# Kernel optimization log

Hardware: AMD Instinct MI355X
Metric: run time of the kernel (lower is better)

Reference implementation:

```python
import jax, jax.numpy as jnp
import numpy as np

DIM = 1024
HEADS = 16

def setup_inputs() -> dict:
    key = jax.random.key(0)
    k1, k2 = jax.random.split(key)
    x = jax.random.normal(k1, (4, 2048, DIM), dtype=jnp.float32)
    # torch nn.Linear(dim, 3*dim, bias=False): weight shape [3*dim, dim], y = x @ W.T
    W_qkv = jax.random.normal(k2, (3 * DIM, DIM), dtype=jnp.float32) * (DIM ** -0.5)
    return {"x": x, "W_qkv": W_qkv}

def reference(x, W_qkv):
    B, N, D = x.shape
    H = HEADS
    hd = D // H
    scale = hd ** -0.5
    qkv = jnp.einsum('bnd,ed->bne', x, W_qkv)            # [B,N,3D]
    qkv = qkv.reshape(B, N, 3, H, hd).transpose(2, 0, 3, 1, 4)  # [3,B,H,N,hd]
    q, k, v = qkv[0], qkv[1], qkv[2]
    attn = jnp.einsum('bhnd,bhmd->bhnm', q, k) * scale   # [B,H,N,N]
    attn = jax.nn.softmax(attn, axis=-1)                 # dropout is identity at eval
    out = jnp.einsum('bhnm,bhmd->bhnd', attn, v)         # [B,H,N,hd]
    return out.transpose(0, 2, 1, 3).reshape(B, N, D)
```

## Files before the change

kernel.cpp:

```cpp
#include <hip/hip_runtime.h>

typedef unsigned short ushort_t;
typedef short bf16x8 __attribute__((ext_vector_type(8)));
typedef float f32x4 __attribute__((ext_vector_type(4)));
typedef float f32x16 __attribute__((ext_vector_type(16)));

__device__ __forceinline__ unsigned f2bf(float f) {
  union { float f; unsigned u; } v; v.f = f;
  return (v.u + 0x7FFFu + ((v.u >> 16) & 1u)) >> 16;
}

__device__ __forceinline__ void gll16(const void* g, const void* l) {
  __builtin_amdgcn_global_load_lds(
      (const __attribute__((address_space(1))) void*)g,
      (__attribute__((address_space(3))) void*)l, 16, 0, 0);
}

__global__ __launch_bounds__(256) void cvt_bf16(const float* __restrict__ src,
                                                ushort_t* __restrict__ dst, int n4) {
  int i = blockIdx.x * 256 + threadIdx.x;
  if (i >= n4) return;
  float4 v = ((const float4*)src)[i];
  uint2 o;
  o.x = f2bf(v.x) | (f2bf(v.y) << 16);
  o.y = f2bf(v.z) | (f2bf(v.w) << 16);
  ((uint2*)dst)[i] = o;
}

__global__ __launch_bounds__(256) void gemm_qkv(const ushort_t* __restrict__ A,
                                                const ushort_t* __restrict__ Bw,
                                                ushort_t* __restrict__ C) {
  __shared__ ushort_t As[128 * 64];
  __shared__ ushort_t Bs[128 * 64];
  const int tid = threadIdx.x;
  const int w = tid >> 6, ln = tid & 63;
  const int g = ln >> 4, lr = ln & 15;
  const int bx = blockIdx.x;
  const int nt = bx % 24, mt = bx / 24;
  const int m0 = mt * 128, n0 = nt * 128;
  const int wr = w >> 1, wc = w & 1;
  const float cscale = (nt < 8) ? 0.18033688f : 1.0f;

  f32x4 acc[4][4] = {};

  for (int kt = 0; kt < 16; ++kt) {
#pragma unroll
    for (int q = 0; q < 4; ++q) {
      int chunk = w * 256 + q * 64 + ln;
      int r = chunk >> 3, c = chunk & 7;
      int cs = c ^ (r & 7);
      gll16(A + (size_t)(m0 + r) * 1024 + kt * 64 + cs * 8, As + chunk * 8);
      gll16(Bw + (size_t)(n0 + r) * 1024 + kt * 64 + cs * 8, Bs + chunk * 8);
    }
    __syncthreads();
#pragma unroll
    for (int ks = 0; ks < 2; ++ks) {
      bf16x8 af[4], bfr[4];
#pragma unroll
      for (int mi = 0; mi < 4; ++mi) {
        int row = wr * 64 + mi * 16 + lr;
        af[mi] = *(const bf16x8*)((const char*)As + row * 128 +
                                  ((g * 16 + ks * 64) ^ ((row & 7) << 4)));
      }
#pragma unroll
      for (int ni = 0; ni < 4; ++ni) {
        int row = wc * 64 + ni * 16 + lr;
        bfr[ni] = *(const bf16x8*)((const char*)Bs + row * 128 +
                                   ((g * 16 + ks * 64) ^ ((row & 7) << 4)));
      }
#pragma unroll
      for (int mi = 0; mi < 4; ++mi)
#pragma unroll
        for (int ni = 0; ni < 4; ++ni)
          acc[mi][ni] = __builtin_amdgcn_mfma_f32_16x16x32_bf16(af[mi], bfr[ni],
                                                                acc[mi][ni], 0, 0, 0);
    }
    __syncthreads();
  }

#pragma unroll
  for (int mi = 0; mi < 4; ++mi)
#pragma unroll
    for (int ni = 0; ni < 4; ++ni)
#pragma unroll
      for (int r = 0; r < 4; ++r) {
        int row = m0 + wr * 64 + mi * 16 + g * 4 + r;
        int col = n0 + wc * 64 + ni * 16 + lr;
        C[(size_t)row * 3072 + col] = (ushort_t)f2bf(acc[mi][ni][r] * cscale);
      }
}

__global__ __launch_bounds__(256) void vtrans(const ushort_t* __restrict__ qkv,
                                              ushort_t* __restrict__ VT) {
  __shared__ ushort_t tl[64][72];
  int blk = blockIdx.x;
  int bh = blk >> 5, nb = blk & 31;
  int b = bh >> 4, h = bh & 15;
  int t = threadIdx.x;
  int r = t >> 2, c = t & 3;
  const ushort_t* src = qkv + (size_t)(b * 2048 + nb * 64 + r) * 3072 + 2048 + h * 64 + c * 16;
  uint2 v0 = *(const uint2*)(src);
  uint2 v1 = *(const uint2*)(src + 4);
  uint2 v2 = *(const uint2*)(src + 8);
  uint2 v3 = *(const uint2*)(src + 12);
  *(uint2*)&tl[r][c * 16] = v0;
  *(uint2*)&tl[r][c * 16 + 4] = v1;
  *(uint2*)&tl[r][c * 16 + 8] = v2;
  *(uint2*)&tl[r][c * 16 + 12] = v3;
  __syncthreads();
  int d = t >> 2, dc = t & 3;
  unsigned pk[8];
#pragma unroll
  for (int j = 0; j < 8; ++j) {
    unsigned lo = tl[dc * 16 + 2 * j][d];
    unsigned hi = tl[dc * 16 + 2 * j + 1][d];
    pk[j] = lo | (hi << 16);
  }
  ushort_t* dst = VT + (size_t)(bh * 64 + d) * 2048 + nb * 64 + dc * 16;
  uint4 o0; o0.x = pk[0]; o0.y = pk[1]; o0.z = pk[4]; o0.w = pk[5];
  uint4 o1; o1.x = pk[2]; o1.y = pk[3]; o1.z = pk[6]; o1.w = pk[7];
  *(uint4*)dst = o0;
  *(uint4*)(dst + 8) = o1;
}

#define SUBTILE(KSB, VSB, LSOUT)                                              \
  {                                                                           \
    const ushort_t* KB = (KSB);                                               \
    const ushort_t* VB = (VSB);                                               \
    f32x16 S;                                                                 \
    _Pragma("unroll") for (int i = 0; i < 16; ++i) S[i] = 0.f;                \
    __builtin_amdgcn_s_setprio(1);                                            \
    _Pragma("unroll") for (int m = 0; m < 4; ++m) {                           \
      bf16x8 kf = *(const bf16x8*)(KB + q * 64 + (((2 * m + h) ^ qsw) * 8));  \
      S = __builtin_amdgcn_mfma_f32_32x32x16_bf16(kf, qf[m], S, 0, 0, 0);     \
    }                                                                         \
    __builtin_amdgcn_s_setprio(0);                                            \
    float p[16];                                                              \
    _Pragma("unroll") for (int i = 0; i < 16; ++i)                            \
      p[i] = __builtin_amdgcn_exp2f(S[i]);                                    \
    float s0 = (p[0] + p[1]) + (p[2] + p[3]);                                 \
    float s1 = (p[4] + p[5]) + (p[6] + p[7]);                                 \
    float s2 = (p[8] + p[9]) + (p[10] + p[11]);                               \
    float s3 = (p[12] + p[13]) + (p[14] + p[15]);                             \
    LSOUT = (s0 + s1) + (s2 + s3);                                            \
    union { unsigned u[4]; bf16x8 v; } pf0, pf1;                              \
    _Pragma("unroll") for (int i = 0; i < 4; ++i)                             \
      asm("v_cvt_pk_bf16_f32 %0, %1, %2"                                      \
          : "=v"(pf0.u[i]) : "v"(p[2 * i]), "v"(p[2 * i + 1]));               \
    _Pragma("unroll") for (int i = 0; i < 4; ++i)                             \
      asm("v_cvt_pk_bf16_f32 %0, %1, %2"                                      \
          : "=v"(pf1.u[i]) : "v"(p[8 + 2 * i]), "v"(p[8 + 2 * i + 1]));       \
    bf16x8 vf0 = *(const bf16x8*)(VB + q * 64 + (((0 + h) ^ qsw) * 8));       \
    bf16x8 vf1 = *(const bf16x8*)(VB + q * 64 + (((2 + h) ^ qsw) * 8));       \
    bf16x8 vf2 = *(const bf16x8*)(VB + q * 64 + (((4 + h) ^ qsw) * 8));       \
    bf16x8 vf3 = *(const bf16x8*)(VB + q * 64 + (((6 + h) ^ qsw) * 8));       \
    __builtin_amdgcn_s_setprio(1);                                            \
    oacc0 = __builtin_amdgcn_mfma_f32_32x32x16_bf16(vf0, pf0.v, oacc0, 0, 0, 0); \
    oacc0 = __builtin_amdgcn_mfma_f32_32x32x16_bf16(vf1, pf1.v, oacc0, 0, 0, 0); \
    oacc1 = __builtin_amdgcn_mfma_f32_32x32x16_bf16(vf2, pf0.v, oacc1, 0, 0, 0); \
    oacc1 = __builtin_amdgcn_mfma_f32_32x32x16_bf16(vf3, pf1.v, oacc1, 0, 0, 0); \
    __builtin_amdgcn_s_setprio(0);                                            \
  }

__global__ __launch_bounds__(256, 4) void attn2(const ushort_t* __restrict__ qkv,
                                                const ushort_t* __restrict__ VT,
                                                float* __restrict__ out) {
  __shared__ ushort_t Ks[3][4096];
  __shared__ ushort_t Vs[3][4096];
  const int blk = blockIdx.x;
  const int bh = blk & 63, qt = blk >> 6;
  const int b = bh >> 4, hh = bh & 15;
  const int tid = threadIdx.x;
  const int w = tid >> 6, l = tid & 63;
  const int q = l & 31, h = l >> 5;
  const int q0 = qt * 128 + w * 32;
  const int qsw = q & 7;

  const ushort_t* qrow = qkv + (size_t)(b * 2048 + q0 + q) * 3072 + hh * 64 + 8 * h;
  bf16x8 qf[4];
#pragma unroll
  for (int m = 0; m < 4; ++m) qf[m] = *(const bf16x8*)(qrow + 16 * m);

  const int rS = tid >> 3, cS = tid & 7;
  const int cL = cS ^ (rS & 7);
  const ushort_t* srcK =
      qkv + (size_t)(b * 2048 + rS) * 3072 + 1024 + hh * 64 + cL * 8;
  const ushort_t* srcV =
      VT + (size_t)(bh * 64 + rS + 32 * (cL >> 2)) * 2048 + (cL & 3) * 8;

  f32x16 oacc0, oacc1;
#pragma unroll
  for (int i = 0; i < 16; ++i) { oacc0[i] = 0.f; oacc1[i] = 0.f; }
  float l_run = 0.f;

  gll16(srcK, Ks[0] + tid * 8);
  gll16(srcK + (size_t)32 * 3072, Ks[0] + 2048 + tid * 8);
  gll16(srcV, Vs[0] + tid * 8);
  gll16(srcV + 32, Vs[0] + 2048 + tid * 8);
  gll16(srcK + (size_t)64 * 3072, Ks[1] + tid * 8);
  gll16(srcK + (size_t)96 * 3072, Ks[1] + 2048 + tid * 8);
  gll16(srcV + 64, Vs[1] + tid * 8);
  gll16(srcV + 96, Vs[1] + 2048 + tid * 8);
  asm volatile("s_waitcnt vmcnt(4)" ::: "memory");
  __builtin_amdgcn_s_barrier();

  int cur = 0;
  for (int tt = 0; tt < 32; ++tt) {
    int tn = tt + 2; if (tn > 31) tn = 31;
    int bufn = cur + 2; if (bufn >= 3) bufn -= 3;
    gll16(srcK + (size_t)(2 * tn) * 32 * 3072, Ks[bufn] + tid * 8);
    gll16(srcK + (size_t)(2 * tn + 1) * 32 * 3072, Ks[bufn] + 2048 + tid * 8);
    gll16(srcV + (2 * tn) * 32, Vs[bufn] + tid * 8);
    gll16(srcV + (2 * tn + 1) * 32, Vs[bufn] + 2048 + tid * 8);

    float ls0, ls1;
    SUBTILE(Ks[cur], Vs[cur], ls0);
    SUBTILE(Ks[cur] + 2048, Vs[cur] + 2048, ls1);
    float ls = ls0 + ls1;
    ls += __shfl_xor(ls, 32, 64);
    l_run += ls;

    asm volatile("s_waitcnt vmcnt(4)" ::: "memory");
    __builtin_amdgcn_s_barrier();
    cur += 1; if (cur == 3) cur = 0;
  }

  float inv = 1.0f / l_run;
  float* orow = out + (size_t)(b * 2048 + q0 + q) * 1024 + hh * 64 + 4 * h;
#pragma unroll
  for (int rq = 0; rq < 4; ++rq) {
    float4 o0, o1;
    o0.x = oacc0[rq * 4 + 0] * inv; o0.y = oacc0[rq * 4 + 1] * inv;
    o0.z = oacc0[rq * 4 + 2] * inv; o0.w = oacc0[rq * 4 + 3] * inv;
    o1.x = oacc1[rq * 4 + 0] * inv; o1.y = oacc1[rq * 4 + 1] * inv;
    o1.z = oacc1[rq * 4 + 2] * inv; o1.w = oacc1[rq * 4 + 3] * inv;
    *(float4*)(orow + 8 * rq) = o0;
    *(float4*)(orow + 32 + 8 * rq) = o1;
  }
}

extern "C" void kernel_launch(void* const* d_in, const int* in_sizes, int n_in,
                              void* d_out, int out_size, void* d_ws, size_t ws_size,
                              hipStream_t stream) {
  const float* x = (const float*)d_in[0];
  const float* Wq = (const float*)d_in[1];
  float* out = (float*)d_out;
  char* ws = (char*)d_ws;

  ushort_t* xb = (ushort_t*)ws;
  ushort_t* wb = (ushort_t*)(ws + 16777216);
  ushort_t* qkv = (ushort_t*)(ws + 23068672);
  ushort_t* VT = xb;

  cvt_bf16<<<8192, 256, 0, stream>>>(x, xb, 8192 * 1024 / 4);
  cvt_bf16<<<3072, 256, 0, stream>>>(Wq, wb, 3072 * 1024 / 4);
  gemm_qkv<<<64 * 24, 256, 0, stream>>>(xb, wb, qkv);
  vtrans<<<64 * 32, 256, 0, stream>>>(qkv, VT);
  attn2<<<64 * 16, 256, 0, stream>>>(qkv, VT, out);
}
```

Baseline: 184.5 us.

## Double attention block to 512 threads covering 256 queries, split K/V loads

The attention kernel now runs 512 threads per block, handling 256 query rows per block instead of 128. Each staged K/V tile is therefore reused by twice as many waves, which halves global K/V traffic per query. The first 256 threads load K and the other 256 load V, so each thread issues two async loads per iteration instead of four, and the vmcnt waits are adjusted to match. The trade-offs are half as many blocks in the grid (512), which may leave CUs underfilled, and the loss of the explicit occupancy hint in launch_bounds.

```diff
diff --git a/kernel.cpp b/kernel.cpp
--- a/kernel.cpp
+++ b/kernel.cpp
@@ -162,9 +162,9 @@
     __builtin_amdgcn_s_setprio(0);                                            \
   }
 
-__global__ __launch_bounds__(256, 4) void attn2(const ushort_t* __restrict__ qkv,
-                                                const ushort_t* __restrict__ VT,
-                                                float* __restrict__ out) {
+__global__ __launch_bounds__(512) void attn2(const ushort_t* __restrict__ qkv,
+                                             const ushort_t* __restrict__ VT,
+                                             float* __restrict__ out) {
   __shared__ ushort_t Ks[3][4096];
   __shared__ ushort_t Vs[3][4096];
   const int blk = blockIdx.x;
@@ -173,7 +173,7 @@
   const int tid = threadIdx.x;
   const int w = tid >> 6, l = tid & 63;
   const int q = l & 31, h = l >> 5;
-  const int q0 = qt * 128 + w * 32;
+  const int q0 = qt * 256 + w * 32;
   const int qsw = q & 7;
 
   const ushort_t* qrow = qkv + (size_t)(b * 2048 + q0 + q) * 3072 + hh * 64 + 8 * h;
@@ -181,37 +181,35 @@
 #pragma unroll
   for (int m = 0; m < 4; ++m) qf[m] = *(const bf16x8*)(qrow + 16 * m);
 
-  const int rS = tid >> 3, cS = tid & 7;
+  const int st = tid & 255;
+  const int rS = st >> 3, cS = st & 7;
   const int cL = cS ^ (rS & 7);
-  const ushort_t* srcK =
-      qkv + (size_t)(b * 2048 + rS) * 3072 + 1024 + hh * 64 + cL * 8;
-  const ushort_t* srcV =
-      VT + (size_t)(bh * 64 + rS + 32 * (cL >> 2)) * 2048 + (cL & 3) * 8;
+  const bool isK = tid < 256;
+  const ushort_t* gsrc =
+      isK ? qkv + (size_t)(b * 2048 + rS) * 3072 + 1024 + hh * 64 + cL * 8
+          : VT + (size_t)(bh * 64 + rS + 32 * (cL >> 2)) * 2048 + (cL & 3) * 8;
+  const size_t gstep = isK ? (size_t)64 * 3072 : (size_t)64;
+  const size_t ghalf = isK ? (size_t)32 * 3072 : (size_t)32;
+  ushort_t* lbase = isK ? &Ks[0][0] : &Vs[0][0];
 
   f32x16 oacc0, oacc1;
 #pragma unroll
   for (int i = 0; i < 16; ++i) { oacc0[i] = 0.f; oacc1[i] = 0.f; }
   float l_run = 0.f;
 
-  gll16(srcK, Ks[0] + tid * 8);
-  gll16(srcK + (size_t)32 * 3072, Ks[0] + 2048 + tid * 8);
-  gll16(srcV, Vs[0] + tid * 8);
-  gll16(srcV + 32, Vs[0] + 2048 + tid * 8);
-  gll16(srcK + (size_t)64 * 3072, Ks[1] + tid * 8);
-  gll16(srcK + (size_t)96 * 3072, Ks[1] + 2048 + tid * 8);
-  gll16(srcV + 64, Vs[1] + tid * 8);
-  gll16(srcV + 96, Vs[1] + 2048 + tid * 8);
-  asm volatile("s_waitcnt vmcnt(4)" ::: "memory");
+  gll16(gsrc, lbase + st * 8);
+  gll16(gsrc + ghalf, lbase + 2048 + st * 8);
+  gll16(gsrc + gstep, lbase + 4096 + st * 8);
+  gll16(gsrc + gstep + ghalf, lbase + 4096 + 2048 + st * 8);
+  asm volatile("s_waitcnt vmcnt(2)" ::: "memory");
   __builtin_amdgcn_s_barrier();
 
   int cur = 0;
   for (int tt = 0; tt < 32; ++tt) {
     int tn = tt + 2; if (tn > 31) tn = 31;
     int bufn = cur + 2; if (bufn >= 3) bufn -= 3;
-    gll16(srcK + (size_t)(2 * tn) * 32 * 3072, Ks[bufn] + tid * 8);
-    gll16(srcK + (size_t)(2 * tn + 1) * 32 * 3072, Ks[bufn] + 2048 + tid * 8);
-    gll16(srcV + (2 * tn) * 32, Vs[bufn] + tid * 8);
-    gll16(srcV + (2 * tn + 1) * 32, Vs[bufn] + 2048 + tid * 8);
+    gll16(gsrc + (size_t)tn * gstep, lbase + bufn * 4096 + st * 8);
+    gll16(gsrc + (size_t)tn * gstep + ghalf, lbase + bufn * 4096 + 2048 + st * 8);
 
     float ls0, ls1;
     SUBTILE(Ks[cur], Vs[cur], ls0);
@@ -220,7 +218,7 @@
     ls += __shfl_xor(ls, 32, 64);
     l_run += ls;
 
-    asm volatile("s_waitcnt vmcnt(4)" ::: "memory");
+    asm volatile("s_waitcnt vmcnt(2)" ::: "memory");
     __builtin_amdgcn_s_barrier();
     cur += 1; if (cur == 3) cur = 0;
   }
@@ -256,5 +254,5 @@
   cvt_bf16<<<3072, 256, 0, stream>>>(Wq, wb, 3072 * 1024 / 4);
   gemm_qkv<<<64 * 24, 256, 0, stream>>>(xb, wb, qkv);
   vtrans<<<64 * 32, 256, 0, stream>>>(qkv, VT);
-  attn2<<<64 * 16, 256, 0, stream>>>(qkv, VT, out);
-}
+  attn2<<<64 * 8, 512, 0, stream>>>(qkv, VT, out);
+}
```

Result: faster. 172.4 us (-6.6%).
